# Kernel tuning notes

Measured on AMD Instinct MI355X. Metric: run time of the kernel, lower is better.

The kernel has to match this reference:

```python
import jax, jax.numpy as jnp
import numpy as np
import math

B, N, EPG = 128, 512, 8192            # graphs, nodes/graph, edges/graph
E = B * EPG
DIN, H, DOUT = 128, 128, 10
RATIO = 0.8
K1 = math.ceil(RATIO * N)             # 410 nodes/graph after pool 1
K2 = math.ceil(RATIO * K1)            # 328 nodes/graph after pool 2
EPS = 1e-5


def setup_inputs() -> dict:
    key = jax.random.key(0)
    ks = jax.random.split(key, 16)
    x = jax.random.normal(ks[0], (B * N, DIN), jnp.float32)
    gid = jnp.repeat(jnp.arange(B, dtype=jnp.int32), EPG)
    src = jax.random.randint(ks[1], (E,), 0, N, dtype=jnp.int32) + gid * N
    dst = jax.random.randint(ks[2], (E,), 0, N, dtype=jnp.int32) + gid * N
    edge_index = jnp.stack([src, dst])

    def w(k, shape, fan_in):
        return jax.random.uniform(k, shape, jnp.float32, -1.0, 1.0) / np.sqrt(fan_in).astype(np.float32)

    return {
        "x": x, "edge_index": edge_index,
        "conv1_W": w(ks[3], (DIN, H), DIN), "conv1_b": jnp.zeros((H,), jnp.float32),
        "conv2_W": w(ks[4], (H, H), H),     "conv2_b": jnp.zeros((H,), jnp.float32),
        "score1_W": w(ks[5], (H, 1), H),    "score1_b": jnp.zeros((1,), jnp.float32),
        "score2_W": w(ks[6], (H, 1), H),    "score2_b": jnp.zeros((1,), jnp.float32),
        "bn1_g": jnp.ones((H,), jnp.float32), "bn1_b": jnp.zeros((H,), jnp.float32),
        "bn1_m": 0.1 * jax.random.normal(ks[7], (H,), jnp.float32),
        "bn1_v": jax.random.uniform(ks[8], (H,), jnp.float32, 0.5, 1.5),
        "bn2_g": jnp.ones((H,), jnp.float32), "bn2_b": jnp.zeros((H,), jnp.float32),
        "bn2_m": 0.1 * jax.random.normal(ks[9], (H,), jnp.float32),
        "bn2_v": jax.random.uniform(ks[10], (H,), jnp.float32, 0.5, 1.5),
        "lin0_W": w(ks[11], (DOUT, DIN), DIN), "lin0_b": jnp.zeros((DOUT,), jnp.float32),
        "lin1_W": w(ks[12], (DOUT, H), H),     "lin1_b": jnp.zeros((DOUT,), jnp.float32),
        "lin2_W": w(ks[13], (DOUT, H), H),     "lin2_b": jnp.zeros((DOUT,), jnp.float32),
    }


def gcn(h_in, src, dst, emask, W, b, n):
    # PyG GCNConv: self-loops + symmetric normalization D^-1/2 (A+I) D^-1/2 (XW) + b
    deg = jnp.ones((n,), h_in.dtype).at[dst].add(emask)      # self-loop counts as 1
    dinv = jax.lax.rsqrt(deg)
    coef = (dinv[src] * dinv[dst] * emask)[:, None]          # masked-out edges -> 0
    h = h_in @ W
    agg = jnp.zeros_like(h).at[dst].add(h[src] * coef)
    return agg + h * (dinv * dinv)[:, None] + b              # self-loop message + bias


def sag_pool(x, score, src, dst, emask, n_per, k):
    # topk per graph (equal-sized graphs -> static shapes), x <- x[perm]*tanh(score[perm])
    idx = jax.lax.top_k(score.reshape(B, n_per), k)[1]                      # [B,k]
    perm = (idx.astype(jnp.int32) + (jnp.arange(B, dtype=jnp.int32) * n_per)[:, None]).reshape(-1)
    xn = x[perm] * jnp.tanh(score[perm])[:, None]
    # filter_adj: remap surviving nodes, mask edges touching dropped nodes
    remap = jnp.full((B * n_per,), -1, jnp.int32).at[perm].set(jnp.arange(B * k, dtype=jnp.int32))
    s2, d2 = remap[src], remap[dst]
    em2 = emask * (s2 >= 0).astype(emask.dtype) * (d2 >= 0).astype(emask.dtype)
    return xn, jnp.maximum(s2, 0), jnp.maximum(d2, 0), em2


def bn_relu(x, g, b, m, v):
    # eval-mode BatchNorm1d followed by ReLU
    return jax.nn.relu(g * (x - m) * jax.lax.rsqrt(v + EPS) + b)


def reference(x, edge_index, conv1_W, conv1_b, conv2_W, conv2_b,
              score1_W, score1_b, score2_W, score2_b,
              bn1_g, bn1_b, bn1_m, bn1_v, bn2_g, bn2_b, bn2_m, bn2_v,
              lin0_W, lin0_b, lin1_W, lin1_b, lin2_W, lin2_b):
    src, dst = edge_index[0], edge_index[1]
    emask = jnp.ones((E,), x.dtype)
    hidden = [(x, N)]
    # layer 0: GCNConv -> SAGPool -> BN -> ReLU
    h = gcn(x, src, dst, emask, conv1_W, conv1_b, B * N)
    s = gcn(h, src, dst, emask, score1_W, score1_b, B * N)[:, 0]
    h, src, dst, emask = sag_pool(h, s, src, dst, emask, N, K1)
    h = bn_relu(h, bn1_g, bn1_b, bn1_m, bn1_v)
    hidden.append((h, K1))
    # layer 1
    h = gcn(h, src, dst, emask, conv2_W, conv2_b, B * K1)
    s = gcn(h, src, dst, emask, score2_W, score2_b, B * K1)[:, 0]
    h, src, dst, emask = sag_pool(h, s, src, dst, emask, K1, K2)
    h = bn_relu(h, bn2_g, bn2_b, bn2_m, bn2_v)
    hidden.append((h, K2))
    # jumping-knowledge readout: global_add_pool each rep, per-layer linear, sum (dropout eval = id)
    lins = [(lin0_W, lin0_b), (lin1_W, lin1_b), (lin2_W, lin2_b)]
    out = jnp.zeros((B, DOUT), x.dtype)
    for (hh, n_per), (W, bb) in zip(hidden, lins):
        pooled = hh.reshape(B, n_per, -1).sum(axis=1)   # global_add_pool (segment sum)
        out = out + pooled @ W.T + bb
    return out
```

## Files before the change

### kernel.cpp

```cpp
#include <hip/hip_runtime.h>

#define Bg   128
#define NPG  512
#define EPGc 8192
#define Etot (Bg*EPGc)
#define DOUTc 10
#define K1c  410
#define K2c  328
#define N0c  (Bg*NPG)
#define N1c  (Bg*K1c)
#define N2c  (Bg*K2c)
#define EPSc 1e-5f

typedef __attribute__((ext_vector_type(8))) short s8v;
typedef __attribute__((ext_vector_type(4))) float f4v;

static __device__ __forceinline__ unsigned short bf_rne(float x) {
  unsigned u = __float_as_uint(x);
  u += 0x7FFFu + ((u >> 16) & 1u);
  return (unsigned short)(u >> 16);
}
static __device__ __forceinline__ float bf_f(unsigned short h) {
  return __uint_as_float(((unsigned)h) << 16);
}

static __global__ __launch_bounds__(512) void k_prep0(const int* __restrict__ src,
                                                      const int* __restrict__ dst,
                                                      const float* __restrict__ W1,
                                                      const float* __restrict__ W2,
                                                      const float* __restrict__ bn1g,
                                                      const float* __restrict__ bn1b,
                                                      const float* __restrict__ bn1m,
                                                      const float* __restrict__ bn1v,
                                                      unsigned short* __restrict__ pk,
                                                      float2* __restrict__ bnp,
                                                      float* __restrict__ dinv,
                                                      int* __restrict__ rp,
                                                      int2* __restrict__ e2,
                                                      float* __restrict__ pooled) {
  __shared__ int    cnt[NPG];
  __shared__ float  sdv[NPG];
  __shared__ int    srp[NPG];
  __shared__ int    sbuf[512];
  int g = blockIdx.x, tid = threadIdx.x;
  cnt[tid] = 0;
  if (tid < 128) {
    pooled[g * 128 + tid] = 0.f;
    pooled[Bg * 128 + g * 128 + tid] = 0.f;
    pooled[2 * Bg * 128 + g * 128 + tid] = 0.f;
    float sc = bn1g[tid] / sqrtf(bn1v[tid] + EPSc);
    bnp[tid] = make_float2(sc, bn1b[tid] - bn1m[tid] * sc);
  }
  if (tid < 256) {
    int i = g * 256 + tid;
    const float* W = (i < 16384) ? W1 : W2;
    unsigned short* d = pk + ((i < 16384) ? 0 : 32768);
    int ii = i & 16383;
    int grp = ii >> 9, lane = (ii >> 3) & 63, j = ii & 7;
    int kk = grp >> 3, t = grp & 7;
    int k = kk * 32 + (lane >> 4) * 8 + j;
    int n = t * 16 + (lane & 15);
    float w = W[k * 128 + n];
    unsigned short hi = bf_rne(w);
    d[ii] = hi;
    d[16384 + ii] = bf_rne(w - bf_f(hi));
  }
  __syncthreads();
  const int* sp = src + (size_t)g * EPGc;
  const int* dp = dst + (size_t)g * EPGc;
  for (int e = tid; e < EPGc; e += 512) atomicAdd(&cnt[dp[e] - g * NPG], 1);
  __syncthreads();
  int c = cnt[tid];
  float dv = 1.0f / sqrtf(1.0f + (float)c);
  sdv[tid] = dv;
  dinv[g * NPG + tid] = dv;
  sbuf[tid] = c;
  __syncthreads();
  for (int off = 1; off < 512; off <<= 1) {
    int t = (tid >= off) ? sbuf[tid - off] : 0;
    __syncthreads();
    sbuf[tid] += t;
    __syncthreads();
  }
  srp[tid] = sbuf[tid] - c;
  rp[g * (NPG + 1) + tid] = sbuf[tid] - c;
  if (tid == 511) rp[g * (NPG + 1) + NPG] = sbuf[511];
  cnt[tid] = 0;
  __syncthreads();
  for (int e = tid; e < EPGc; e += 512) {
    int s = sp[e], d = dp[e];
    int dl = d - g * NPG;
    int pos = srp[dl] + atomicAdd(&cnt[dl], 1);
    e2[(size_t)g * EPGc + pos] =
        make_int2(s, __float_as_int(sdv[s - g * NPG] * sdv[dl]));
  }
}

template <bool FUSE, int NROWG>
static __global__ __launch_bounds__(512) void k_gemm4(const float* __restrict__ X,
                                                      const unsigned short* __restrict__ pk,
                                                      float* __restrict__ Y,
                                                      float* __restrict__ pooledseg,
                                                      const int* __restrict__ perm,
                                                      const float* __restrict__ tsel,
                                                      const float2* __restrict__ bnp) {
  __shared__ unsigned short wl[32768];
  int tid = threadIdx.x;
  for (int i = tid; i < 4096; i += 512) ((int4*)wl)[i] = ((const int4*)pk)[i];
  int wv = tid >> 6, lane = tid & 63;
  int q = lane >> 4, m16 = lane & 15;
  int grow0 = blockIdx.x * 128 + wv * 16;
  int row = grow0 + m16;
  int gsel = row / NROWG;
  bool uni = (grow0 / NROWG) == ((grow0 + 15) / NROWG);
  const float* xr_base;
  float tmul = 1.f;
  if (FUSE) {
    int old = perm[row];
    tmul = tsel[row];
    xr_base = X + (size_t)old * 128;
  } else {
    xr_base = X + (size_t)row * 128;
  }
  s8v ahi[4], alo[4];
#pragma unroll
  for (int kk = 0; kk < 4; ++kk) {
    const float* xr = xr_base + kk * 32 + q * 8;
    float4 a0 = *(const float4*)xr;
    float4 a1 = *(const float4*)(xr + 4);
    float av[8] = {a0.x, a0.y, a0.z, a0.w, a1.x, a1.y, a1.z, a1.w};
    if (FUSE) {
#pragma unroll
      for (int j = 0; j < 8; ++j) {
        float2 ss = bnp[kk * 32 + q * 8 + j];
        av[j] = fmaxf(ss.x * (av[j] * tmul) + ss.y, 0.f);
      }
    }
    if (pooledseg) {
      if (uni) {
#pragma unroll
        for (int j = 0; j < 8; ++j) {
          float v = av[j];
          v += __shfl_xor(v, 1, 64); v += __shfl_xor(v, 2, 64);
          v += __shfl_xor(v, 4, 64); v += __shfl_xor(v, 8, 64);
          if (m16 == 0) atomicAdd(&pooledseg[gsel * 128 + kk * 32 + q * 8 + j], v);
        }
      } else {
#pragma unroll
        for (int j = 0; j < 8; ++j)
          atomicAdd(&pooledseg[gsel * 128 + kk * 32 + q * 8 + j], av[j]);
      }
    }
    union { unsigned short u[8]; s8v v; } H, L;
#pragma unroll
    for (int j = 0; j < 8; ++j) {
      unsigned short h = bf_rne(av[j]);
      H.u[j] = h;
      L.u[j] = bf_rne(av[j] - bf_f(h));
    }
    ahi[kk] = H.v; alo[kk] = L.v;
  }
  __syncthreads();
  int orow0 = grow0 + q * 4;
#pragma unroll
  for (int t = 0; t < 8; ++t) {
    f4v acc = {0.f, 0.f, 0.f, 0.f};
#pragma unroll
    for (int kk = 0; kk < 4; ++kk) {
      s8v bhi = *(const s8v*)&wl[(kk * 8 + t) * 512 + lane * 8];
      s8v blo = *(const s8v*)&wl[16384 + (kk * 8 + t) * 512 + lane * 8];
      acc = __builtin_amdgcn_mfma_f32_16x16x32_bf16(ahi[kk], bhi, acc, 0, 0, 0);
      acc = __builtin_amdgcn_mfma_f32_16x16x32_bf16(alo[kk], bhi, acc, 0, 0, 0);
      acc = __builtin_amdgcn_mfma_f32_16x16x32_bf16(ahi[kk], blo, acc, 0, 0, 0);
    }
#pragma unroll
    for (int r = 0; r < 4; ++r)
      Y[(size_t)(orow0 + r) * 128 + t * 16 + m16] = acc[r];
  }
}

template <int NPER, int RG>
static __global__ __launch_bounds__(256) void k_agg3(const float* __restrict__ h0,
                                                     const float* __restrict__ dinv,
                                                     const float* __restrict__ bias,
                                                     const int* __restrict__ rp,
                                                     const int2* __restrict__ e2,
                                                     const float* __restrict__ sw,
                                                     float* __restrict__ h1,
                                                     float* __restrict__ spre) {
  int tid = threadIdx.x;
  int hw = tid >> 5, l = tid & 31;
  int b = blockIdx.x;
  int xcd = b & 7, slot = b >> 3;
  int g = xcd * 16 + (slot & 15);
  int rowgrp = slot >> 4;
  int li = rowgrp * 8 + hw;
  if (li >= NPER) return;
  int j = g * NPER + li;
  const int* rpg = rp + g * (NPER + 1);
  int start = rpg[li], end = rpg[li + 1];
  const int2* ep = e2 + (size_t)g * EPGc;
  float di = dinv[j];
  float sc = di * di;
  float4 acc = *(const float4*)&h0[(size_t)j * 128 + l * 4];
  float4 bb = ((const float4*)bias)[l];
  acc.x = acc.x * sc + bb.x; acc.y = acc.y * sc + bb.y;
  acc.z = acc.z * sc + bb.z; acc.w = acc.w * sc + bb.w;
  int e = start;
  for (; e + 4 <= end; e += 4) {
    int2 p0 = ep[e], p1 = ep[e + 1], p2 = ep[e + 2], p3 = ep[e + 3];
    float4 v0 = *(const float4*)&h0[(size_t)p0.x * 128 + l * 4];
    float4 v1 = *(const float4*)&h0[(size_t)p1.x * 128 + l * 4];
    float4 v2 = *(const float4*)&h0[(size_t)p2.x * 128 + l * 4];
    float4 v3 = *(const float4*)&h0[(size_t)p3.x * 128 + l * 4];
    float c0 = __int_as_float(p0.y), c1 = __int_as_float(p1.y);
    float c2 = __int_as_float(p2.y), c3 = __int_as_float(p3.y);
    acc.x += v0.x * c0 + v1.x * c1 + v2.x * c2 + v3.x * c3;
    acc.y += v0.y * c0 + v1.y * c1 + v2.y * c2 + v3.y * c3;
    acc.z += v0.z * c0 + v1.z * c1 + v2.z * c2 + v3.z * c3;
    acc.w += v0.w * c0 + v1.w * c1 + v2.w * c2 + v3.w * c3;
  }
  for (; e < end; ++e) {
    int2 pp = ep[e];
    float c = __int_as_float(pp.y);
    float4 v = *(const float4*)&h0[(size_t)pp.x * 128 + l * 4];
    acc.x += v.x * c; acc.y += v.y * c; acc.z += v.z * c; acc.w += v.w * c;
  }
  ((float4*)&h1[(size_t)j * 128])[l] = acc;
  float4 w4 = ((const float4*)sw)[l];
  float pr = acc.x * w4.x + acc.y * w4.y + acc.z * w4.z + acc.w * w4.w;
#pragma unroll
  for (int off = 16; off; off >>= 1) pr += __shfl_xor(pr, off, 64);
  if (l == 0) spre[j] = pr;
}

template <int NPER, int K>
static __global__ __launch_bounds__(512) void k_repool(const float* __restrict__ spre,
                                                       const float* __restrict__ dinv,
                                                       const float* __restrict__ sb,
                                                       const int* __restrict__ rp,
                                                       const int* __restrict__ src,
                                                       const int* __restrict__ dst,
                                                       int* __restrict__ perm,
                                                       float* __restrict__ tsel,
                                                       float* __restrict__ dinv2,
                                                       int* __restrict__ rp2,
                                                       int2* __restrict__ e2) {
  __shared__ float ss[NPER];
  __shared__ float sc[512];
  __shared__ int   sidx[512];
  __shared__ short rmp[NPER];
  __shared__ int   cnt[K];
  __shared__ float sdv[K];
  __shared__ int   srp[K];
  __shared__ int   sbuf[512];
  int g = blockIdx.x, tid = threadIdx.x;
  if (tid < NPER) { ss[tid] = spre[g * NPER + tid]; rmp[tid] = -1; }
  __syncthreads();
  if (tid < NPER) {
    const int* rpg = rp + g * (NPER + 1);
    int st = rpg[tid], en = rpg[tid + 1];
    const int2* ep = e2 + (size_t)g * EPGc;
    float di = dinv[g * NPER + tid];
    float acc = ss[tid] * di * di + sb[0];
    int e = st;
    for (; e + 4 <= en; e += 4) {
      int2 p0 = ep[e], p1 = ep[e + 1], p2 = ep[e + 2], p3 = ep[e + 3];
      acc += ss[p0.x - g * NPER] * __int_as_float(p0.y) +
             ss[p1.x - g * NPER] * __int_as_float(p1.y) +
             ss[p2.x - g * NPER] * __int_as_float(p2.y) +
             ss[p3.x - g * NPER] * __int_as_float(p3.y);
    }
    for (; e < en; ++e) { int2 pp = ep[e]; acc += ss[pp.x - g * NPER] * __int_as_float(pp.y); }
    sc[tid] = acc;
  } else {
    sc[tid] = -3.402823466e38f;
  }
  sidx[tid] = tid;
  __syncthreads();
  for (int kk = 2; kk <= 512; kk <<= 1) {
    for (int j = kk >> 1; j > 0; j >>= 1) {
      int i = tid, p = i ^ j;
      if (p > i) {
        bool up = ((i & kk) == 0);
        float si = sc[i], sp2 = sc[p];
        if (up ? (si < sp2) : (si > sp2)) {
          sc[i] = sp2; sc[p] = si;
          int t = sidx[i]; sidx[i] = sidx[p]; sidx[p] = t;
        }
      }
      __syncthreads();
    }
  }
  if (tid < K) {
    perm[g * K + tid] = g * NPER + sidx[tid];
    tsel[g * K + tid] = tanhf(sc[tid]);
    rmp[sidx[tid]] = (short)tid;
    cnt[tid] = 0;
  }
  __syncthreads();
  const int* sp = src + (size_t)g * EPGc;
  const int* dp = dst + (size_t)g * EPGc;
  for (int e = tid; e < EPGc; e += 512) {
    int s = rmp[sp[e] - g * NPER];
    int d = rmp[dp[e] - g * NPER];
    if ((s | d) >= 0) atomicAdd(&cnt[d], 1);
  }
  __syncthreads();
  int c = (tid < K) ? cnt[tid] : 0;
  if (tid < K) {
    float dv = 1.0f / sqrtf(1.0f + (float)c);
    sdv[tid] = dv;
    dinv2[g * K + tid] = dv;
  }
  sbuf[tid] = c;
  __syncthreads();
  for (int off = 1; off < 512; off <<= 1) {
    int t = (tid >= off) ? sbuf[tid - off] : 0;
    __syncthreads();
    sbuf[tid] += t;
    __syncthreads();
  }
  if (tid < K) { srp[tid] = sbuf[tid] - c; rp2[g * (K + 1) + tid] = sbuf[tid] - c; cnt[tid] = 0; }
  if (tid == 511) rp2[g * (K + 1) + K] = sbuf[511];
  __syncthreads();
  for (int e = tid; e < EPGc; e += 512) {
    int s = rmp[sp[e] - g * NPER];
    int d = rmp[dp[e] - g * NPER];
    if ((s | d) >= 0) {
      int pos = srp[d] + atomicAdd(&cnt[d], 1);
      e2[(size_t)g * EPGc + pos] = make_int2(g * K + s, __float_as_int(sdv[s] * sdv[d]));
    }
  }
}

template <int NPER, int K>
static __global__ __launch_bounds__(512) void k_topk2(const float* __restrict__ spre,
                                                      const float* __restrict__ dinv2,
                                                      const float* __restrict__ sb,
                                                      const int* __restrict__ rp2,
                                                      const int2* __restrict__ e2,
                                                      int* __restrict__ perm,
                                                      float* __restrict__ tsel) {
  __shared__ float ss[NPER];
  __shared__ float sc[512];
  __shared__ int   sidx[512];
  int g = blockIdx.x, tid = threadIdx.x;
  if (tid < NPER) ss[tid] = spre[g * NPER + tid];
  __syncthreads();
  if (tid < NPER) {
    const int* rpg = rp2 + g * (NPER + 1);
    int st = rpg[tid], en = rpg[tid + 1];
    const int2* ep = e2 + (size_t)g * EPGc;
    float di = dinv2[g * NPER + tid];
    float acc = ss[tid] * di * di + sb[0];
    int e = st;
    for (; e + 4 <= en; e += 4) {
      int2 p0 = ep[e], p1 = ep[e + 1], p2 = ep[e + 2], p3 = ep[e + 3];
      acc += ss[p0.x - g * NPER] * __int_as_float(p0.y) +
             ss[p1.x - g * NPER] * __int_as_float(p1.y) +
             ss[p2.x - g * NPER] * __int_as_float(p2.y) +
             ss[p3.x - g * NPER] * __int_as_float(p3.y);
    }
    for (; e < en; ++e) { int2 pp = ep[e]; acc += ss[pp.x - g * NPER] * __int_as_float(pp.y); }
    sc[tid] = acc;
  } else {
    sc[tid] = -3.402823466e38f;
  }
  sidx[tid] = tid;
  __syncthreads();
  for (int kk = 2; kk <= 512; kk <<= 1) {
    for (int j = kk >> 1; j > 0; j >>= 1) {
      int i = tid, p = i ^ j;
      if (p > i) {
        bool up = ((i & kk) == 0);
        float si = sc[i], sp2 = sc[p];
        if (up ? (si < sp2) : (si > sp2)) {
          sc[i] = sp2; sc[p] = si;
          int t = sidx[i]; sidx[i] = sidx[p]; sidx[p] = t;
        }
      }
      __syncthreads();
    }
  }
  if (tid < K) {
    perm[g * K + tid] = g * NPER + sidx[tid];
    tsel[g * K + tid] = tanhf(sc[tid]);
  }
}

template <int NPER, int CH>
static __global__ __launch_bounds__(128) void k_poolbn(const float* __restrict__ h,
                                                       const float* __restrict__ tsel,
                                                       const int* __restrict__ perm,
                                                       const float* __restrict__ gg,
                                                       const float* __restrict__ bb,
                                                       const float* __restrict__ mm,
                                                       const float* __restrict__ vv,
                                                       float* __restrict__ pooledseg) {
  int g = blockIdx.x / CH, cidx = blockIdx.x - g * CH;
  int f = threadIdx.x;
  const int rows = (NPER + CH - 1) / CH;
  int r0 = cidx * rows, r1 = min(NPER, r0 + rows);
  if (r0 >= r1) return;
  float G = gg[f], Bb = bb[f], Mm = mm[f];
  float inv = 1.0f / sqrtf(vv[f] + EPSc);
  float acc = 0.f;
  for (int r = r0; r < r1; ++r) {
    int j = g * NPER + r;
    int old = perm[j];
    float val = h[(size_t)old * 128 + f] * tsel[j];
    float o = fmaxf(G * (val - Mm) * inv + Bb, 0.f);
    acc += o;
  }
  atomicAdd(&pooledseg[g * 128 + f], acc);
}

static __global__ void k_final(const float* __restrict__ pooled,
                               const float* __restrict__ w0, const float* __restrict__ b0,
                               const float* __restrict__ w1, const float* __restrict__ b1,
                               const float* __restrict__ w2, const float* __restrict__ b2,
                               float* __restrict__ out) {
  int t = blockIdx.x * 256 + threadIdx.x;
  if (t >= Bg * DOUTc) return;
  int g = t / DOUTc, o = t - g * DOUTc;
  const float* p0 = pooled + g * 128;
  const float* p1 = pooled + Bg * 128 + g * 128;
  const float* p2 = pooled + 2 * Bg * 128 + g * 128;
  float acc = b0[o] + b1[o] + b2[o];
  for (int k = 0; k < 128; ++k)
    acc += p0[k] * w0[o * 128 + k] + p1[k] * w1[o * 128 + k] + p2[k] * w2[o * 128 + k];
  out[t] = acc;
}

extern "C" void kernel_launch(void* const* d_in, const int* in_sizes, int n_in,
                              void* d_out, int out_size, void* d_ws, size_t ws_size,
                              hipStream_t stream) {
  (void)in_sizes; (void)n_in; (void)out_size; (void)ws_size;
  const float* x    = (const float*)d_in[0];
  const int*   ei   = (const int*)d_in[1];
  const int*   src0 = ei;
  const int*   dst0 = ei + Etot;
  const float* c1W = (const float*)d_in[2];  const float* c1b = (const float*)d_in[3];
  const float* c2W = (const float*)d_in[4];  const float* c2b = (const float*)d_in[5];
  const float* s1W = (const float*)d_in[6];  const float* s1b = (const float*)d_in[7];
  const float* s2W = (const float*)d_in[8];  const float* s2b = (const float*)d_in[9];
  const float* bn1g = (const float*)d_in[10]; const float* bn1b = (const float*)d_in[11];
  const float* bn1m = (const float*)d_in[12]; const float* bn1v = (const float*)d_in[13];
  const float* bn2g = (const float*)d_in[14]; const float* bn2b = (const float*)d_in[15];
  const float* bn2m = (const float*)d_in[16]; const float* bn2v = (const float*)d_in[17];
  const float* l0W = (const float*)d_in[18]; const float* l0b = (const float*)d_in[19];
  const float* l1W = (const float*)d_in[20]; const float* l1b = (const float*)d_in[21];
  const float* l2W = (const float*)d_in[22]; const float* l2b = (const float*)d_in[23];
  float* out = (float*)d_out;

  char* p = (char*)d_ws;
  auto alloc = [&](size_t bytes) { char* q = p; p += (bytes + 255) & ~(size_t)255; return q; };
  float* h0    = (float*)alloc((size_t)N0c * 128 * 4);
  float* h1    = (float*)alloc((size_t)N0c * 128 * 4);
  float* dinv  = (float*)alloc((size_t)N0c * 4);
  float* dinv2 = (float*)alloc((size_t)N1c * 4);
  int*   rp    = (int*)alloc((size_t)Bg * (NPG + 1) * 4);
  int*   rp2   = (int*)alloc((size_t)Bg * (K1c + 1) * 4);
  int2*  e2    = (int2*)alloc((size_t)Etot * 8);
  float* spre  = (float*)alloc((size_t)N0c * 4);
  float* tsel  = (float*)alloc((size_t)N1c * 4);
  int*   perm  = (int*)alloc((size_t)N1c * 4);
  unsigned short* pk = (unsigned short*)alloc((size_t)65536 * 2);
  float2* bnp  = (float2*)alloc((size_t)128 * 8);
  float* pooled= (float*)alloc((size_t)3 * Bg * 128 * 4);

  dim3 b256(256), b512(512), b128(128);

  k_prep0<<<Bg, b512, 0, stream>>>(src0, dst0, c1W, c2W, bn1g, bn1b, bn1m, bn1v,
                                   pk, bnp, dinv, rp, e2, pooled);
  k_gemm4<false, NPG><<<N0c / 128, b512, 0, stream>>>(x, pk, h0, pooled,
                                                      nullptr, nullptr, nullptr);
  k_agg3<NPG, 64><<<128 * 64, b256, 0, stream>>>(h0, dinv, c1b, rp, e2, s1W, h1, spre);
  k_repool<NPG, K1c><<<Bg, b512, 0, stream>>>(spre, dinv, s1b, rp, src0, dst0,
                                              perm, tsel, dinv2, rp2, e2);

  float* g1 = h0;
  k_gemm4<true, K1c><<<N1c / 128, b512, 0, stream>>>(h1, pk + 32768, g1,
                                                     pooled + Bg * 128, perm, tsel, bnp);
  float* h2 = h1;
  k_agg3<K1c, 52><<<128 * 52, b256, 0, stream>>>(g1, dinv2, c2b, rp2, e2, s2W, h2, spre);
  k_topk2<K1c, K2c><<<Bg, b512, 0, stream>>>(spre, dinv2, s2b, rp2, e2, perm, tsel);
  k_poolbn<K2c, 16><<<Bg * 16, b128, 0, stream>>>(h2, tsel, perm, bn2g, bn2b,
                                                  bn2m, bn2v, pooled + 2 * Bg * 128);

  k_final<<<(Bg * DOUTc + 255) / 256, b256, 0, stream>>>(pooled, l0W, l0b, l1W, l1b, l2W, l2b, out);
}
```

Before: 353.8 us.

## Make GEMM kernel persistent with 256-thread blocks and two row-tiles per wave

The GEMM kernel becomes persistent: 512 blocks of 256 threads loop over 128-row tiles, so the 64KB packed weight load into LDS is paid once per block rather than once per tile. Each wave now handles 32 rows (two 16-row sub-tiles), reusing each LDS B fragment for two sets of MFMAs and interleaving independent accumulators to hide MFMA latency. The cost is more registers per thread, lower occupancy given the 64KB LDS footprint, and less latency hiding from fewer waves.

```diff
diff --git a/kernel.cpp b/kernel.cpp
--- a/kernel.cpp
+++ b/kernel.cpp
@@ -97,85 +97,99 @@
 }
 
 template <bool FUSE, int NROWG>
-static __global__ __launch_bounds__(512) void k_gemm4(const float* __restrict__ X,
-                                                      const unsigned short* __restrict__ pk,
-                                                      float* __restrict__ Y,
-                                                      float* __restrict__ pooledseg,
-                                                      const int* __restrict__ perm,
-                                                      const float* __restrict__ tsel,
-                                                      const float2* __restrict__ bnp) {
+static __global__ __launch_bounds__(256, 2) void k_gemm7(const float* __restrict__ X,
+                                                         const unsigned short* __restrict__ pk,
+                                                         float* __restrict__ Y,
+                                                         float* __restrict__ pooledseg,
+                                                         const int* __restrict__ perm,
+                                                         const float* __restrict__ tsel,
+                                                         const float2* __restrict__ bnp,
+                                                         int ntiles) {
   __shared__ unsigned short wl[32768];
   int tid = threadIdx.x;
-  for (int i = tid; i < 4096; i += 512) ((int4*)wl)[i] = ((const int4*)pk)[i];
+  for (int i = tid; i < 4096; i += 256) ((int4*)wl)[i] = ((const int4*)pk)[i];
+  __syncthreads();
   int wv = tid >> 6, lane = tid & 63;
   int q = lane >> 4, m16 = lane & 15;
-  int grow0 = blockIdx.x * 128 + wv * 16;
-  int row = grow0 + m16;
-  int gsel = row / NROWG;
-  bool uni = (grow0 / NROWG) == ((grow0 + 15) / NROWG);
-  const float* xr_base;
-  float tmul = 1.f;
-  if (FUSE) {
-    int old = perm[row];
-    tmul = tsel[row];
-    xr_base = X + (size_t)old * 128;
-  } else {
-    xr_base = X + (size_t)row * 128;
-  }
-  s8v ahi[4], alo[4];
-#pragma unroll
-  for (int kk = 0; kk < 4; ++kk) {
-    const float* xr = xr_base + kk * 32 + q * 8;
-    float4 a0 = *(const float4*)xr;
-    float4 a1 = *(const float4*)(xr + 4);
-    float av[8] = {a0.x, a0.y, a0.z, a0.w, a1.x, a1.y, a1.z, a1.w};
-    if (FUSE) {
-#pragma unroll
-      for (int j = 0; j < 8; ++j) {
-        float2 ss = bnp[kk * 32 + q * 8 + j];
-        av[j] = fmaxf(ss.x * (av[j] * tmul) + ss.y, 0.f);
+  for (int tile = blockIdx.x; tile < ntiles; tile += gridDim.x) {
+    int base = tile * 128 + wv * 32;
+    s8v ahi[2][4], alo[2][4];
+#pragma unroll
+    for (int s = 0; s < 2; ++s) {
+      int grow0 = base + s * 16;
+      int row = grow0 + m16;
+      int gsel = row / NROWG;
+      bool uni = (grow0 / NROWG) == ((grow0 + 15) / NROWG);
+      const float* xr_base;
+      float tmul = 1.f;
+      if (FUSE) {
+        int old = perm[row];
+        tmul = tsel[row];
+        xr_base = X + (size_t)old * 128;
+      } else {
+        xr_base = X + (size_t)row * 128;
       }
-    }
-    if (pooledseg) {
-      if (uni) {
+#pragma unroll
+      for (int kk = 0; kk < 4; ++kk) {
+        const float* xr = xr_base + kk * 32 + q * 8;
+        float4 a0 = *(const float4*)xr;
+        float4 a1 = *(const float4*)(xr + 4);
+        float av[8] = {a0.x, a0.y, a0.z, a0.w, a1.x, a1.y, a1.z, a1.w};
+        if (FUSE) {
+#pragma unroll
+          for (int j = 0; j < 8; ++j) {
+            float2 ss = bnp[kk * 32 + q * 8 + j];
+            av[j] = fmaxf(ss.x * (av[j] * tmul) + ss.y, 0.f);
+          }
+        }
+        if (pooledseg) {
+          if (uni) {
+#pragma unroll
+            for (int j = 0; j < 8; ++j) {
+              float v = av[j];
+              v += __shfl_xor(v, 1, 64); v += __shfl_xor(v, 2, 64);
+              v += __shfl_xor(v, 4, 64); v += __shfl_xor(v, 8, 64);
+              if (m16 == 0) atomicAdd(&pooledseg[gsel * 128 + kk * 32 + q * 8 + j], v);
+            }
+          } else {
+#pragma unroll
+            for (int j = 0; j < 8; ++j)
+              atomicAdd(&pooledseg[gsel * 128 + kk * 32 + q * 8 + j], av[j]);
+          }
+        }
+        union { unsigned short u[8]; s8v v; } H, L;
 #pragma unroll
         for (int j = 0; j < 8; ++j) {
-          float v = av[j];
-          v += __shfl_xor(v, 1, 64); v += __shfl_xor(v, 2, 64);
-          v += __shfl_xor(v, 4, 64); v += __shfl_xor(v, 8, 64);
-          if (m16 == 0) atomicAdd(&pooledseg[gsel * 128 + kk * 32 + q * 8 + j], v);
+          unsigned short h = bf_rne(av[j]);
+          H.u[j] = h;
+          L.u[j] = bf_rne(av[j] - bf_f(h));
         }
-      } else {
-#pragma unroll
-        for (int j = 0; j < 8; ++j)
-          atomicAdd(&pooledseg[gsel * 128 + kk * 32 + q * 8 + j], av[j]);
+        ahi[s][kk] = H.v; alo[s][kk] = L.v;
       }
     }
-    union { unsigned short u[8]; s8v v; } H, L;
-#pragma unroll
-    for (int j = 0; j < 8; ++j) {
-      unsigned short h = bf_rne(av[j]);
-      H.u[j] = h;
-      L.u[j] = bf_rne(av[j] - bf_f(h));
-    }
-    ahi[kk] = H.v; alo[kk] = L.v;
-  }
-  __syncthreads();
-  int orow0 = grow0 + q * 4;
-#pragma unroll
-  for (int t = 0; t < 8; ++t) {
-    f4v acc = {0.f, 0.f, 0.f, 0.f};
-#pragma unroll
-    for (int kk = 0; kk < 4; ++kk) {
-      s8v bhi = *(const s8v*)&wl[(kk * 8 + t) * 512 + lane * 8];
-      s8v blo = *(const s8v*)&wl[16384 + (kk * 8 + t) * 512 + lane * 8];
-      acc = __builtin_amdgcn_mfma_f32_16x16x32_bf16(ahi[kk], bhi, acc, 0, 0, 0);
-      acc = __builtin_amdgcn_mfma_f32_16x16x32_bf16(alo[kk], bhi, acc, 0, 0, 0);
-      acc = __builtin_amdgcn_mfma_f32_16x16x32_bf16(ahi[kk], blo, acc, 0, 0, 0);
-    }
-#pragma unroll
-    for (int r = 0; r < 4; ++r)
-      Y[(size_t)(orow0 + r) * 128 + t * 16 + m16] = acc[r];
+#pragma unroll
+    for (int t = 0; t < 8; ++t) {
+      f4v acc0 = {0.f, 0.f, 0.f, 0.f};
+      f4v acc1 = {0.f, 0.f, 0.f, 0.f};
+#pragma unroll
+      for (int kk = 0; kk < 4; ++kk) {
+        s8v bhi = *(const s8v*)&wl[(kk * 8 + t) * 512 + lane * 8];
+        s8v blo = *(const s8v*)&wl[16384 + (kk * 8 + t) * 512 + lane * 8];
+        acc0 = __builtin_amdgcn_mfma_f32_16x16x32_bf16(ahi[0][kk], bhi, acc0, 0, 0, 0);
+        acc1 = __builtin_amdgcn_mfma_f32_16x16x32_bf16(ahi[1][kk], bhi, acc1, 0, 0, 0);
+        acc0 = __builtin_amdgcn_mfma_f32_16x16x32_bf16(alo[0][kk], bhi, acc0, 0, 0, 0);
+        acc1 = __builtin_amdgcn_mfma_f32_16x16x32_bf16(alo[1][kk], bhi, acc1, 0, 0, 0);
+        acc0 = __builtin_amdgcn_mfma_f32_16x16x32_bf16(ahi[0][kk], blo, acc0, 0, 0, 0);
+        acc1 = __builtin_amdgcn_mfma_f32_16x16x32_bf16(ahi[1][kk], blo, acc1, 0, 0, 0);
+      }
+      int o0 = base + q * 4;
+      int o1 = base + 16 + q * 4;
+#pragma unroll
+      for (int r = 0; r < 4; ++r) {
+        Y[(size_t)(o0 + r) * 128 + t * 16 + m16] = acc0[r];
+        Y[(size_t)(o1 + r) * 128 + t * 16 + m16] = acc1[r];
+      }
+    }
   }
 }
 
@@ -474,15 +488,16 @@
 
   k_prep0<<<Bg, b512, 0, stream>>>(src0, dst0, c1W, c2W, bn1g, bn1b, bn1m, bn1v,
                                    pk, bnp, dinv, rp, e2, pooled);
-  k_gemm4<false, NPG><<<N0c / 128, b512, 0, stream>>>(x, pk, h0, pooled,
-                                                      nullptr, nullptr, nullptr);
+  k_gemm7<false, NPG><<<512, b256, 0, stream>>>(x, pk, h0, pooled,
+                                                nullptr, nullptr, nullptr, N0c / 128);
   k_agg3<NPG, 64><<<128 * 64, b256, 0, stream>>>(h0, dinv, c1b, rp, e2, s1W, h1, spre);
   k_repool<NPG, K1c><<<Bg, b512, 0, stream>>>(spre, dinv, s1b, rp, src0, dst0,
                                               perm, tsel, dinv2, rp2, e2);
 
   float* g1 = h0;
-  k_gemm4<true, K1c><<<N1c / 128, b512, 0, stream>>>(h1, pk + 32768, g1,
-                                                     pooled + Bg * 128, perm, tsel, bnp);
+  k_gemm7<true, K1c><<<512, b256, 0, stream>>>(h1, pk + 32768, g1,
+                                               pooled + Bg * 128, perm, tsel, bnp,
+                                               N1c / 128);
   float* h2 = h1;
   k_agg3<K1c, 52><<<128 * 52, b256, 0, stream>>>(g1, dinv2, c2b, rp2, e2, s2W, h2, spre);
   k_topk2<K1c, K2c><<<Bg, b512, 0, stream>>>(spre, dinv2, s2b, rp2, e2, perm, tsel);
```

Measured after the change: 361.5 us. +2.2%, slower.
